# Performance work log

Hardware: AMD Instinct MI355X
Metric: run time of the kernel (lower is better)

## Reference

```python
import jax, jax.numpy as jnp
import numpy as np
from jax import lax

EPS = 1e-12

def _l2norm(v, axis):
    n = jnp.linalg.norm(v, axis=axis, keepdims=True)
    return v / jnp.maximum(n, EPS)

def setup_inputs() -> dict:
    key = jax.random.key(0)
    k1, k2, k3 = jax.random.split(key, 3)
    C, H, W, K = 512, 192, 192, 64
    x = jax.random.normal(k1, (C, H, W), dtype=jnp.float32)
    conv_w = jax.random.normal(k2, (K, C), dtype=jnp.float32) * 0.05  # 1x1 conv, no bias (vladv2=False)
    centroids = jax.random.uniform(k3, (K, C), dtype=jnp.float32)
    return {"x": x, "conv_w": conv_w, "centroids": centroids}

def reference(x, conv_w, centroids):
    K = conv_w.shape[0]
    x4 = x[None]                      # [1,C,H,W]
    N, C, H, W = x4.shape
    L = H * W
    # descriptor-wise L2 normalization over channels
    x4 = _l2norm(x4, axis=1)
    # 1x1 conv -> soft assignment over clusters
    logits = jnp.einsum('kc,nchw->nkhw', conv_w, x4)
    soft = jax.nn.softmax(logits, axis=1)          # [N,K,H,W]
    sa_flat = soft.reshape(N, K, L)
    # top-2 cluster indices per location (argmax + second largest)
    _, top2 = lax.top_k(sa_flat.transpose(0, 2, 1), 2)  # [N,L,2]
    first, second = top2[..., 0], top2[..., 1]
    # unfold 3x3, padding 1: windows [N, L, K, 9] in (kh,kw) order
    pad = jnp.pad(soft, ((0, 0), (0, 0), (1, 1), (1, 1)))
    patches = jnp.stack([pad[:, :, di:di + H, dj:dj + W]
                         for di in range(3) for dj in range(3)], axis=2)  # [N,K,9,H,W]
    windows = patches.reshape(N, K, 9, L).transpose(0, 3, 1, 2)           # [N,L,K,9]
    # keep only windows of the top-2 clusters at each location
    karange = jnp.arange(K)[None, None, :]
    keep = (karange == first[:, :, None]) | (karange == second[:, :, None])  # [N,L,K]
    wsel = windows * keep[..., None].astype(windows.dtype)
    # fold (transpose of unfold): overlap-add back to [N,K,H,W]
    ws = wsel.transpose(0, 2, 3, 1).reshape(N, K, 9, H, W)
    out_pad = jnp.zeros((N, K, H + 2, W + 2), dtype=ws.dtype)
    t = 0
    for di in range(3):
        for dj in range(3):
            out_pad = out_pad.at[:, :, di:di + H, dj:dj + W].add(ws[:, :, t])
            t += 1
    weight = out_pad[:, :, 1:H + 1, 1:W + 1]
    # border mask: (min distance to border)^4
    ii = jnp.arange(H); jj = jnp.arange(W)
    mi = jnp.minimum(H - 1 - ii, ii)[:, None]
    mj = jnp.minimum(W - 1 - jj, jj)[None, :]
    m = jnp.minimum(mi, mj).astype(weight.dtype)
    m2 = m * m
    mask = m2 * m2
    weight = weight * mask[None, None]
    sa2 = weight.reshape(N, K, L)
    # per-cluster residual accumulation, vectorized (replaces the 64-iter loop)
    xf = x4.reshape(N, C, L)
    vlad = jnp.einsum('nkl,ncl->nkc', sa2, xf) - sa2.sum(-1)[..., None] * centroids[None]
    vlad = _l2norm(vlad, axis=2)               # intra-normalization
    v = vlad.reshape(N, -1)
    v = _l2norm(v, axis=1)
    return v
```

## Files before the change

kernel.cpp:

```cpp
#include <hip/hip_runtime.h>

#define HH 192
#define WW 192
#define LL (HH * WW)
#define CC 512
#define KK 64
#define EPSF 1e-12f
typedef unsigned long long ull;
typedef unsigned int uint;
typedef unsigned short ushort;

#define NCHUNK 192
#define CHUNKL (LL / NCHUNK)

typedef short bf16x8 __attribute__((ext_vector_type(8)));
typedef float f32x4 __attribute__((ext_vector_type(4)));

__device__ inline void split3(float v, ushort& h, ushort& md, ushort& lo) {
    uint b  = __float_as_uint(v);
    uint hb = b & 0xFFFF0000u;
    float r1 = v - __uint_as_float(hb);
    uint mb = __float_as_uint(r1) & 0xFFFF0000u;
    float r2 = r1 - __uint_as_float(mb);
    uint lb = __float_as_uint(r2) & 0xFFFF0000u;
    h = (ushort)(hb >> 16); md = (ushort)(mb >> 16); lo = (ushort)(lb >> 16);
}

__global__ __launch_bounds__(256) void k0_prep(const float* __restrict__ w,
                                               ushort* __restrict__ Whi,
                                               ushort* __restrict__ Wmid,
                                               ushort* __restrict__ Wlo,
                                               float* __restrict__ Szero) {
    int idx = blockIdx.x * 256 + threadIdx.x;
    int k = idx >> 9;
    int c = idx & 511;
    int s = c >> 5, w32 = c & 31, quad = w32 >> 3, j = w32 & 7;
    int kg = k >> 4, m = k & 15;
    int dst = (((s * 4 + kg) * 4 + quad) * 16 + m) * 8 + j;
    float v = w[idx];
    ushort h, md, lo;
    split3(v, h, md, lo);
    Whi[dst] = h; Wmid[dst] = md; Wlo[dst] = lo;
    if (blockIdx.x == 0 && threadIdx.x < 128) Szero[threadIdx.x] = 0.f;
}

__global__ __launch_bounds__(128) void k1_logits(const float* __restrict__ x,
                                                 const ushort* __restrict__ Whi,
                                                 const ushort* __restrict__ Wmid,
                                                 const ushort* __restrict__ Wlo,
                                                 float* __restrict__ soft,
                                                 float* __restrict__ invn,
                                                 ull* __restrict__ keep) {
    __shared__ float accL[32][64];
    __shared__ float ssL[2][64];
    int t = threadIdx.x, lane = t & 63, wid = t >> 6;
    int m = lane & 15, quad = lane >> 4;
    int pb = blockIdx.x * 32;

    f32x4 acc[4][2];
#pragma unroll
    for (int kg = 0; kg < 4; ++kg)
#pragma unroll
        for (int cg = 0; cg < 2; ++cg) acc[kg][cg] = (f32x4){0.f, 0.f, 0.f, 0.f};
    float ssA[2] = {0.f, 0.f};

    const float* xq = x + (size_t)(wid * 256 + quad * 8) * LL + pb + m;

    float xv[2][8];
#pragma unroll
    for (int j = 0; j < 8; ++j) {
        const float* xr = xq + (size_t)j * LL;
        xv[0][j] = xr[0];
        xv[1][j] = xr[16];
    }

    for (int s = 0; s < 8; ++s) {
        int s16 = wid * 8 + s;
        bf16x8 Ah[4], Am[4], Al[4];
#pragma unroll
        for (int kg = 0; kg < 4; ++kg) {
            size_t off = (size_t)(((s16 * 4 + kg) * 64 + lane) * 8);
            Ah[kg] = *(const bf16x8*)(Whi  + off);
            Am[kg] = *(const bf16x8*)(Wmid + off);
            Al[kg] = *(const bf16x8*)(Wlo  + off);
        }
        float xn[2][8];
        if (s < 7) {
            const float* xq2 = xq + (size_t)32 * LL;
#pragma unroll
            for (int j = 0; j < 8; ++j) {
                const float* xr = xq2 + (size_t)j * LL;
                xn[0][j] = xr[0];
                xn[1][j] = xr[16];
            }
        }
        bf16x8 Bh[2], Bm[2], Bl[2];
#pragma unroll
        for (int cg = 0; cg < 2; ++cg)
#pragma unroll
            for (int j = 0; j < 8; ++j) {
                float v = xv[cg][j];
                ssA[cg] = fmaf(v, v, ssA[cg]);
                ushort h, md, lo;
                split3(v, h, md, lo);
                Bh[cg][j] = (short)h; Bm[cg][j] = (short)md; Bl[cg][j] = (short)lo;
            }
#pragma unroll
        for (int kg = 0; kg < 4; ++kg)
#pragma unroll
            for (int cg = 0; cg < 2; ++cg) {
                f32x4 a = acc[kg][cg];
                a = __builtin_amdgcn_mfma_f32_16x16x32_bf16(Ah[kg], Bh[cg], a, 0, 0, 0);
                a = __builtin_amdgcn_mfma_f32_16x16x32_bf16(Ah[kg], Bm[cg], a, 0, 0, 0);
                a = __builtin_amdgcn_mfma_f32_16x16x32_bf16(Am[kg], Bh[cg], a, 0, 0, 0);
                a = __builtin_amdgcn_mfma_f32_16x16x32_bf16(Ah[kg], Bl[cg], a, 0, 0, 0);
                a = __builtin_amdgcn_mfma_f32_16x16x32_bf16(Al[kg], Bh[cg], a, 0, 0, 0);
                a = __builtin_amdgcn_mfma_f32_16x16x32_bf16(Am[kg], Bm[cg], a, 0, 0, 0);
                acc[kg][cg] = a;
            }
        if (s < 7) {
#pragma unroll
            for (int cg = 0; cg < 2; ++cg)
#pragma unroll
                for (int j = 0; j < 8; ++j) xv[cg][j] = xn[cg][j];
            xq += (size_t)32 * LL;
        }
    }

    if (wid == 1) {
#pragma unroll
        for (int kg = 0; kg < 4; ++kg)
#pragma unroll
            for (int cg = 0; cg < 2; ++cg)
#pragma unroll
                for (int r = 0; r < 4; ++r)
                    accL[kg * 8 + cg * 4 + r][lane] = acc[kg][cg][r];
        ssL[0][lane] = ssA[0];
        ssL[1][lane] = ssA[1];
    }
    __syncthreads();
    if (wid != 0) return;
#pragma unroll
    for (int kg = 0; kg < 4; ++kg)
#pragma unroll
        for (int cg = 0; cg < 2; ++cg)
#pragma unroll
            for (int r = 0; r < 4; ++r)
                acc[kg][cg][r] += accL[kg * 8 + cg * 4 + r][lane];
    ssA[0] += ssL[0][lane];
    ssA[1] += ssL[1][lane];

#pragma unroll
    for (int cg = 0; cg < 2; ++cg) {
        float ssv = ssA[cg];
        ssv += __shfl_xor(ssv, 16);
        ssv += __shfl_xor(ssv, 32);
        float iv = 1.0f / fmaxf(sqrtf(ssv), EPSF);
        int px = pb + cg * 16 + m;
        if (quad == 0) invn[px] = iv;

        float lg[16];
        float M1 = -3.0e38f, M2 = -3.0e38f; int I1 = 0, I2 = 0;
#pragma unroll
        for (int kg = 0; kg < 4; ++kg)
#pragma unroll
            for (int r = 0; r < 4; ++r) {
                float v = acc[kg][cg][r] * iv;
                lg[kg * 4 + r] = v;
                int kk = kg * 16 + quad * 4 + r;
                if (v > M1)      { M2 = M1; I2 = I1; M1 = v; I1 = kk; }
                else if (v > M2) { M2 = v; I2 = kk; }
            }
#pragma unroll
        for (int st = 0; st < 2; ++st) {
            int d = 16 << st;
            float a1 = __shfl_xor(M1, d); int b1 = __shfl_xor(I1, d);
            float a2 = __shfl_xor(M2, d); int b2 = __shfl_xor(I2, d);
            if (a1 > M1 || (a1 == M1 && b1 < I1)) { M2 = M1; I2 = I1; M1 = a1; I1 = b1; }
            else if (a1 > M2 || (a1 == M2 && b1 < I2)) { M2 = a1; I2 = b1; }
            if (a2 > M1 || (a2 == M1 && b2 < I1)) { M2 = M1; I2 = I1; M1 = a2; I1 = b2; }
            else if (a2 > M2 || (a2 == M2 && b2 < I2)) { M2 = a2; I2 = b2; }
        }

        float es = 0.f;
#pragma unroll
        for (int q = 0; q < 16; ++q) { float e = __expf(lg[q] - M1); lg[q] = e; es += e; }
        es += __shfl_xor(es, 16);
        es += __shfl_xor(es, 32);
        float rs = 1.0f / es;

        float4* sp = (float4*)(soft + (size_t)px * KK + quad * 4);
#pragma unroll
        for (int kg = 0; kg < 4; ++kg) {
            float4 o;
            o.x = lg[kg * 4 + 0] * rs; o.y = lg[kg * 4 + 1] * rs;
            o.z = lg[kg * 4 + 2] * rs; o.w = lg[kg * 4 + 3] * rs;
            sp[kg * 4] = o;
        }
        if (quad == 0) keep[px] = (1ull << I1) | (1ull << I2);
    }
}

__global__ __launch_bounds__(256) void k2_weight(float* __restrict__ soft,
                                                 const ull* __restrict__ keep,
                                                 const float* __restrict__ invn,
                                                 float* __restrict__ S) {
    __shared__ float sred[4][64];
    int t = threadIdx.x, lane = t & 63, wid = t >> 6;
    int l0 = blockIdx.x * 32 + wid * 8;
    float sk = 0.f;
#pragma unroll
    for (int p = 0; p < 8; ++p) {
        int l = l0 + p;
        int i = l / WW, j = l % WW;
        int m = min(min(i, HH - 1 - i), min(j, WW - 1 - j));
        float bm = (float)m; bm *= bm; bm *= bm;
        int cnt = 0;
#pragma unroll
        for (int di = -1; di <= 1; ++di) {
            int ii = i + di;
            if (ii < 0 || ii >= HH) continue;
#pragma unroll
            for (int dj = -1; dj <= 1; ++dj) {
                int jj = j + dj;
                if (jj < 0 || jj >= WW) continue;
                ull nb = keep[ii * WW + jj];
                cnt += (int)((nb >> lane) & 1ull);
            }
        }
        float v = soft[(size_t)l * KK + lane];
        float u = v * (float)cnt * bm;
        sk += u;
        soft[(size_t)l * KK + lane] = u * invn[l];
    }
    sred[wid][lane] = sk;
    __syncthreads();
    if (wid == 0)
        atomicAdd(&S[lane], sred[0][lane] + sred[1][lane] + sred[2][lane] + sred[3][lane]);
}

__device__ inline void cvt_pair(float v0, float v1, uint& hp, uint& lp) {
    uint b0 = __float_as_uint(v0), b1 = __float_as_uint(v1);
    uint h0 = b0 & 0xFFFF0000u, h1 = b1 & 0xFFFF0000u;
    float r0 = v0 - __uint_as_float(h0);
    float r1 = v1 - __uint_as_float(h1);
    hp = (h0 >> 16) | h1;
    lp = (__float_as_uint(r0) >> 16) | (__float_as_uint(r1) & 0xFFFF0000u);
}

__global__ __launch_bounds__(256) void k3_mfma(const float* __restrict__ w2,
                                               const float* __restrict__ x,
                                               float* __restrict__ partials) {
    __shared__ ushort wa_hi[64][40], wa_lo[64][40];
    __shared__ ushort xb_hi[128][40], xb_lo[128][40];
    int chunk = blockIdx.x;
    int c0 = blockIdx.y * 128;
    int l0 = chunk * CHUNKL;
    int t = threadIdx.x, lane = t & 63, wid = t >> 6;
    int m = lane & 15, quad = lane >> 4;

    f32x4 acc[4][2];
#pragma unroll
    for (int kg = 0; kg < 4; ++kg)
#pragma unroll
        for (int cg = 0; cg < 2; ++cg) acc[kg][cg] = (f32x4){0.f, 0.f, 0.f, 0.f};

    for (int lb = 0; lb < CHUNKL; lb += 32) {
        {
            int k = t & 63, rg = t >> 6;
#pragma unroll
            for (int i = 0; i < 4; ++i) {
                int lp = rg + 4 * i;
                int gl = l0 + lb + 2 * lp;
                float v0 = w2[(size_t)gl * KK + k];
                float v1 = w2[(size_t)(gl + 1) * KK + k];
                uint hp, lq;
                cvt_pair(v0, v1, hp, lq);
                *(uint*)&wa_hi[k][2 * lp] = hp;
                *(uint*)&wa_lo[k][2 * lp] = lq;
            }
        }
        {
            int lp = t & 15, cb = t >> 4;
            int gl = l0 + lb + 2 * lp;
#pragma unroll
            for (int i = 0; i < 8; ++i) {
                int c = cb + 16 * i;
                float v0 = x[(size_t)(c0 + c) * LL + gl];
                float v1 = x[(size_t)(c0 + c) * LL + gl + 1];
                uint hp, lq;
                cvt_pair(v0, v1, hp, lq);
                *(uint*)&xb_hi[c][2 * lp] = hp;
                *(uint*)&xb_lo[c][2 * lp] = lq;
            }
        }
        __syncthreads();
        bf16x8 Ah[4], Al[4];
#pragma unroll
        for (int kg = 0; kg < 4; ++kg) {
            Ah[kg] = *(bf16x8*)&wa_hi[kg * 16 + m][quad * 8];
            Al[kg] = *(bf16x8*)&wa_lo[kg * 16 + m][quad * 8];
        }
#pragma unroll
        for (int cg = 0; cg < 2; ++cg) {
            int crow = wid * 32 + cg * 16 + m;
            bf16x8 Bh = *(bf16x8*)&xb_hi[crow][quad * 8];
            bf16x8 Bl = *(bf16x8*)&xb_lo[crow][quad * 8];
#pragma unroll
            for (int kg = 0; kg < 4; ++kg) {
                acc[kg][cg] = __builtin_amdgcn_mfma_f32_16x16x32_bf16(Ah[kg], Bh, acc[kg][cg], 0, 0, 0);
                acc[kg][cg] = __builtin_amdgcn_mfma_f32_16x16x32_bf16(Ah[kg], Bl, acc[kg][cg], 0, 0, 0);
                acc[kg][cg] = __builtin_amdgcn_mfma_f32_16x16x32_bf16(Al[kg], Bh, acc[kg][cg], 0, 0, 0);
            }
        }
        __syncthreads();
    }
    float* pp = partials + (size_t)chunk * KK * CC;
#pragma unroll
    for (int kg = 0; kg < 4; ++kg)
#pragma unroll
        for (int cg = 0; cg < 2; ++cg) {
            int cout = c0 + wid * 32 + cg * 16 + m;
#pragma unroll
            for (int r = 0; r < 4; ++r) {
                int kout = kg * 16 + quad * 4 + r;
                pp[(size_t)kout * CC + cout] = acc[kg][cg][r];
            }
        }
}

__global__ __launch_bounds__(512) void k4a_reduce(const float* __restrict__ partials,
                                                  const float* __restrict__ S,
                                                  const float* __restrict__ cent,
                                                  float* __restrict__ vlad,
                                                  float* __restrict__ rowsq) {
    __shared__ float red[512];
    int k = blockIdx.x;
    int ci = threadIdx.x & 127;
    int c = blockIdx.y * 128 + ci;
    int q = threadIdx.x >> 7;
    const float* pk = partials + (size_t)q * (NCHUNK / 4) * KK * CC + (size_t)k * CC + c;
    float s0 = 0.f, s1 = 0.f, s2 = 0.f, s3 = 0.f;
    for (int ch = 0; ch < NCHUNK / 4; ch += 4) {
        s0 += pk[(size_t)(ch + 0) * KK * CC];
        s1 += pk[(size_t)(ch + 1) * KK * CC];
        s2 += pk[(size_t)(ch + 2) * KK * CC];
        s3 += pk[(size_t)(ch + 3) * KK * CC];
    }
    red[threadIdx.x] = (s0 + s1) + (s2 + s3);
    __syncthreads();
    float vsq = 0.f;
    if (q == 0) {
        float v = red[ci] + red[ci + 128] + red[ci + 256] + red[ci + 384];
        v -= S[k] * cent[k * CC + c];
        vlad[k * CC + c] = v;
        vsq = v * v;
    }
    __syncthreads();
    red[threadIdx.x] = vsq;
    __syncthreads();
    for (int off = 256; off > 0; off >>= 1) {
        if (threadIdx.x < off) red[threadIdx.x] += red[threadIdx.x + off];
        __syncthreads();
    }
    if (threadIdx.x == 0) atomicAdd(&rowsq[k], red[0]);
}

__global__ __launch_bounds__(256) void k4c_finish(const float* __restrict__ vlad,
                                                  const float* __restrict__ rowsq,
                                                  float* __restrict__ out) {
    __shared__ float rns[64];
    int t = threadIdx.x;
    if (t < 64) {
        float tot = rowsq[t];
        float r = 1.0f / fmaxf(sqrtf(tot), EPSF);
        float contrib = tot * r * r;
#pragma unroll
        for (int off = 32; off; off >>= 1) contrib += __shfl_xor(contrib, off, 64);
        float ginv = 1.0f / fmaxf(sqrtf(contrib), EPSF);
        rns[t] = r * ginv;
    }
    __syncthreads();
    int idx4 = blockIdx.x * 256 + t;
    int k = idx4 >> 7;
    float s = rns[k];
    float4 v = ((const float4*)vlad)[idx4];
    v.x *= s; v.y *= s; v.z *= s; v.w *= s;
    ((float4*)out)[idx4] = v;
}

extern "C" void kernel_launch(void* const* d_in, const int* in_sizes, int n_in,
                              void* d_out, int out_size, void* d_ws, size_t ws_size,
                              hipStream_t stream) {
    const float* x      = (const float*)d_in[0];
    const float* conv_w = (const float*)d_in[1];
    const float* cent   = (const float*)d_in[2];
    float* out = (float*)d_out;

    float* ws    = (float*)d_ws;
    ushort* Whi  = (ushort*)ws;
    ushort* Wmid = Whi + 32768;
    ushort* Wlo  = Wmid + 32768;
    float* soft  = ws + 49152;
    float* invn  = soft + (size_t)KK * LL;
    float* S     = invn + LL;
    float* rowsq = S + KK;
    float* vlad  = rowsq + KK;
    ull*   keep  = (ull*)(vlad + 32768);
    float* partials = (float*)(keep + LL);

    k0_prep<<<(KK * CC) / 256, 256, 0, stream>>>(conv_w, Whi, Wmid, Wlo, S);
    k1_logits<<<LL / 32, 128, 0, stream>>>(x, Whi, Wmid, Wlo, soft, invn, keep);
    k2_weight<<<LL / 32, 256, 0, stream>>>(soft, keep, invn, S);
    k3_mfma<<<dim3(NCHUNK, 4), 256, 0, stream>>>(soft, x, partials);
    k4a_reduce<<<dim3(KK, 4), 512, 0, stream>>>(partials, S, cent, vlad, rowsq);
    k4c_finish<<<(KK * CC / 4) / 256, 256, 0, stream>>>(vlad, rowsq, out);
}
```

Measured before the change: 196.3 us.

## Split k1 channel reduction over four waves and double-buffer weight/x loads

The logits kernel now runs four waves per block instead of two, so each wave covers 128 channels rather than 256. Partial accumulators from three waves are reduced through LDS by wave 0. The weight fragments and x values for the next step are loaded into a second register buffer while the current step's MFMAs run, and a sched_barrier keeps the prefetch ahead of the compute. This aims to hide global load latency and raise parallelism, at the cost of more registers, more LDS and a larger cross-wave reduction.

```diff
diff --git a/kernel.cpp b/kernel.cpp
--- a/kernel.cpp
+++ b/kernel.cpp
@@ -44,18 +44,19 @@
     if (blockIdx.x == 0 && threadIdx.x < 128) Szero[threadIdx.x] = 0.f;
 }
 
-__global__ __launch_bounds__(128) void k1_logits(const float* __restrict__ x,
+__global__ __launch_bounds__(256) void k1_logits(const float* __restrict__ x,
                                                  const ushort* __restrict__ Whi,
                                                  const ushort* __restrict__ Wmid,
                                                  const ushort* __restrict__ Wlo,
                                                  float* __restrict__ soft,
                                                  float* __restrict__ invn,
                                                  ull* __restrict__ keep) {
-    __shared__ float accL[32][64];
-    __shared__ float ssL[2][64];
+    __shared__ float accL[3][32][64];
+    __shared__ float ssL[3][2][64];
     int t = threadIdx.x, lane = t & 63, wid = t >> 6;
     int m = lane & 15, quad = lane >> 4;
     int pb = blockIdx.x * 32;
+    int s16base = wid * 4;
 
     f32x4 acc[4][2];
 #pragma unroll
@@ -64,42 +65,53 @@
         for (int cg = 0; cg < 2; ++cg) acc[kg][cg] = (f32x4){0.f, 0.f, 0.f, 0.f};
     float ssA[2] = {0.f, 0.f};
 
-    const float* xq = x + (size_t)(wid * 256 + quad * 8) * LL + pb + m;
-
-    float xv[2][8];
+    const float* xq = x + (size_t)(wid * 128 + quad * 8) * LL + pb + m;
+
+    bf16x8 Ah[2][4], Am[2][4], Al[2][4];
+    float xv[2][2][8];
+
+#pragma unroll
+    for (int kg = 0; kg < 4; ++kg) {
+        size_t off = (size_t)(((s16base * 4 + kg) * 64 + lane) * 8);
+        Ah[0][kg] = *(const bf16x8*)(Whi  + off);
+        Am[0][kg] = *(const bf16x8*)(Wmid + off);
+        Al[0][kg] = *(const bf16x8*)(Wlo  + off);
+    }
 #pragma unroll
     for (int j = 0; j < 8; ++j) {
         const float* xr = xq + (size_t)j * LL;
-        xv[0][j] = xr[0];
-        xv[1][j] = xr[16];
-    }
-
-    for (int s = 0; s < 8; ++s) {
-        int s16 = wid * 8 + s;
-        bf16x8 Ah[4], Am[4], Al[4];
-#pragma unroll
-        for (int kg = 0; kg < 4; ++kg) {
-            size_t off = (size_t)(((s16 * 4 + kg) * 64 + lane) * 8);
-            Ah[kg] = *(const bf16x8*)(Whi  + off);
-            Am[kg] = *(const bf16x8*)(Wmid + off);
-            Al[kg] = *(const bf16x8*)(Wlo  + off);
-        }
-        float xn[2][8];
-        if (s < 7) {
-            const float* xq2 = xq + (size_t)32 * LL;
+        xv[0][0][j] = xr[0];
+        xv[0][1][j] = xr[16];
+    }
+
+#pragma unroll
+    for (int s = 0; s < 4; ++s) {
+        const int cur = s & 1, nxt = cur ^ 1;
+        if (s < 3) {
+            int s16 = s16base + s + 1;
+#pragma unroll
+            for (int kg = 0; kg < 4; ++kg) {
+                size_t off = (size_t)(((s16 * 4 + kg) * 64 + lane) * 8);
+                Ah[nxt][kg] = *(const bf16x8*)(Whi  + off);
+                Am[nxt][kg] = *(const bf16x8*)(Wmid + off);
+                Al[nxt][kg] = *(const bf16x8*)(Wlo  + off);
+            }
+            const float* xp = xq + (size_t)(s + 1) * 32 * LL;
 #pragma unroll
             for (int j = 0; j < 8; ++j) {
-                const float* xr = xq2 + (size_t)j * LL;
-                xn[0][j] = xr[0];
-                xn[1][j] = xr[16];
-            }
-        }
+                const float* xr = xp + (size_t)j * LL;
+                xv[nxt][0][j] = xr[0];
+                xv[nxt][1][j] = xr[16];
+            }
+        }
+        __builtin_amdgcn_sched_barrier(0);
+
         bf16x8 Bh[2], Bm[2], Bl[2];
 #pragma unroll
         for (int cg = 0; cg < 2; ++cg)
 #pragma unroll
             for (int j = 0; j < 8; ++j) {
-                float v = xv[cg][j];
+                float v = xv[cur][cg][j];
                 ssA[cg] = fmaf(v, v, ssA[cg]);
                 ushort h, md, lo;
                 split3(v, h, md, lo);
@@ -110,45 +122,41 @@
 #pragma unroll
             for (int cg = 0; cg < 2; ++cg) {
                 f32x4 a = acc[kg][cg];
-                a = __builtin_amdgcn_mfma_f32_16x16x32_bf16(Ah[kg], Bh[cg], a, 0, 0, 0);
-                a = __builtin_amdgcn_mfma_f32_16x16x32_bf16(Ah[kg], Bm[cg], a, 0, 0, 0);
-                a = __builtin_amdgcn_mfma_f32_16x16x32_bf16(Am[kg], Bh[cg], a, 0, 0, 0);
-                a = __builtin_amdgcn_mfma_f32_16x16x32_bf16(Ah[kg], Bl[cg], a, 0, 0, 0);
-                a = __builtin_amdgcn_mfma_f32_16x16x32_bf16(Al[kg], Bh[cg], a, 0, 0, 0);
-                a = __builtin_amdgcn_mfma_f32_16x16x32_bf16(Am[kg], Bm[cg], a, 0, 0, 0);
+                a = __builtin_amdgcn_mfma_f32_16x16x32_bf16(Ah[cur][kg], Bh[cg], a, 0, 0, 0);
+                a = __builtin_amdgcn_mfma_f32_16x16x32_bf16(Ah[cur][kg], Bm[cg], a, 0, 0, 0);
+                a = __builtin_amdgcn_mfma_f32_16x16x32_bf16(Am[cur][kg], Bh[cg], a, 0, 0, 0);
+                a = __builtin_amdgcn_mfma_f32_16x16x32_bf16(Ah[cur][kg], Bl[cg], a, 0, 0, 0);
+                a = __builtin_amdgcn_mfma_f32_16x16x32_bf16(Al[cur][kg], Bh[cg], a, 0, 0, 0);
+                a = __builtin_amdgcn_mfma_f32_16x16x32_bf16(Am[cur][kg], Bm[cg], a, 0, 0, 0);
                 acc[kg][cg] = a;
             }
-        if (s < 7) {
+    }
+
+    if (wid != 0) {
+#pragma unroll
+        for (int kg = 0; kg < 4; ++kg)
 #pragma unroll
             for (int cg = 0; cg < 2; ++cg)
 #pragma unroll
-                for (int j = 0; j < 8; ++j) xv[cg][j] = xn[cg][j];
-            xq += (size_t)32 * LL;
-        }
-    }
-
-    if (wid == 1) {
+                for (int r = 0; r < 4; ++r)
+                    accL[wid - 1][kg * 8 + cg * 4 + r][lane] = acc[kg][cg][r];
+        ssL[wid - 1][0][lane] = ssA[0];
+        ssL[wid - 1][1][lane] = ssA[1];
+    }
+    __syncthreads();
+    if (wid != 0) return;
+#pragma unroll
+    for (int q = 0; q < 3; ++q) {
 #pragma unroll
         for (int kg = 0; kg < 4; ++kg)
 #pragma unroll
             for (int cg = 0; cg < 2; ++cg)
 #pragma unroll
                 for (int r = 0; r < 4; ++r)
-                    accL[kg * 8 + cg * 4 + r][lane] = acc[kg][cg][r];
-        ssL[0][lane] = ssA[0];
-        ssL[1][lane] = ssA[1];
-    }
-    __syncthreads();
-    if (wid != 0) return;
-#pragma unroll
-    for (int kg = 0; kg < 4; ++kg)
-#pragma unroll
-        for (int cg = 0; cg < 2; ++cg)
-#pragma unroll
-            for (int r = 0; r < 4; ++r)
-                acc[kg][cg][r] += accL[kg * 8 + cg * 4 + r][lane];
-    ssA[0] += ssL[0][lane];
-    ssA[1] += ssL[1][lane];
+                    acc[kg][cg][r] += accL[q][kg * 8 + cg * 4 + r][lane];
+        ssA[0] += ssL[q][0][lane];
+        ssA[1] += ssL[q][1][lane];
+    }
 
 #pragma unroll
     for (int cg = 0; cg < 2; ++cg) {
@@ -410,7 +418,7 @@
     float* partials = (float*)(keep + LL);
 
     k0_prep<<<(KK * CC) / 256, 256, 0, stream>>>(conv_w, Whi, Wmid, Wlo, S);
-    k1_logits<<<LL / 32, 128, 0, stream>>>(x, Whi, Wmid, Wlo, soft, invn, keep);
+    k1_logits<<<LL / 32, 256, 0, stream>>>(x, Whi, Wmid, Wlo, soft, invn, keep);
     k2_weight<<<LL / 32, 256, 0, stream>>>(soft, keep, invn, S);
     k3_mfma<<<dim3(NCHUNK, 4), 256, 0, stream>>>(soft, x, partials);
     k4a_reduce<<<dim3(KK, 4), 512, 0, stream>>>(partials, S, cent, vlad, rowsq);
```

After: 198.7 us. No clear change (+1.2%).
